# Kernel tuning notes

Measured on AMD Instinct MI355X. Metric: run time of the kernel, lower is better.

The kernel has to match this reference:

```python
import jax, jax.numpy as jnp
import numpy as np

B, S, D, H = 2, 2048, 1024, 16
HD = D // H  # head_dim = 64


def setup_inputs() -> dict:
    key = jax.random.key(0)
    ks = jax.random.split(key, 9)
    s = 1.0 / np.sqrt(D)
    return {
        "x": jax.random.normal(ks[0], (B, S, D), dtype=jnp.float32),
        "Wq": jax.random.uniform(ks[1], (D, D), jnp.float32, -s, s),
        "bq": jnp.zeros((D,), jnp.float32),
        "Wk": jax.random.uniform(ks[2], (D, D), jnp.float32, -s, s),
        "bk": jnp.zeros((D,), jnp.float32),
        "Wv": jax.random.uniform(ks[3], (D, D), jnp.float32, -s, s),
        "bv": jnp.zeros((D,), jnp.float32),
        "Wo": jax.random.uniform(ks[4], (D, D), jnp.float32, -s, s),
        "bo": jnp.zeros((D,), jnp.float32),
    }


def reference(x, Wq, bq, Wk, bk, Wv, bv, Wo, bo):
    # x: [B,S,D] -> Q/K/V: [B,H,S,HD]
    def heads(t):
        return t.reshape(B, S, H, HD).transpose(0, 2, 1, 3)

    Q = heads(x @ Wq + bq)
    K = heads(x @ Wk + bk)
    V = heads(x @ Wv + bv)
    scale = jnp.sqrt(jnp.asarray(HD, dtype=x.dtype))
    energy = jnp.einsum("bhqd,bhkd->bhqk", Q, K) / scale  # [B,H,S,S]
    attn = jax.nn.softmax(energy, axis=-1)
    # dropout is identity in eval mode
    o = jnp.einsum("bhqk,bhkd->bhqd", attn, V)  # [B,H,S,HD]
    o = o.transpose(0, 2, 1, 3).reshape(B, S, D)
    return o @ Wo + bo
```

## Files before the change

kernel.cpp:

```cpp
#include <hip/hip_runtime.h>
#include <hip/hip_bf16.h>

#define B_  2
#define S_  2048
#define D_  1024
#define H_  16
#define HD_ 64

typedef __attribute__((ext_vector_type(8))) short bf16x8;
typedef __attribute__((ext_vector_type(4))) float f32x4;

typedef __attribute__((address_space(1))) const short gbl_short;
typedef __attribute__((address_space(3))) short lds_short;

__device__ __forceinline__ short f2bf(float f) {
  union { float f; unsigned u; } v; v.f = f;
  unsigned r = (v.u + 0x7FFFu + ((v.u >> 16) & 1u)) >> 16;
  return (short)r;
}

__device__ __forceinline__ short bf16s(float f) {
  __hip_bfloat16 h = __float2bfloat16(f);
  return *reinterpret_cast<short*>(&h);
}

__global__ __launch_bounds__(256) void cast_x_kernel(const float* __restrict__ x,
                                                     short* __restrict__ xb) {
  int i = blockIdx.x * 256 + threadIdx.x;
  float4 v = ((const float4*)x)[i];
  short4 o;
  o.x = f2bf(v.x); o.y = f2bf(v.y); o.z = f2bf(v.z); o.w = f2bf(v.w);
  ((short4*)xb)[i] = o;
}

__global__ __launch_bounds__(256) void transpose_cast_w(
    const float* __restrict__ w0, const float* __restrict__ w1,
    const float* __restrict__ w2, const float* __restrict__ w3,
    short* __restrict__ t0, short* __restrict__ t1,
    short* __restrict__ t2, short* __restrict__ t3) {
  const float* W = blockIdx.z == 0 ? w0 : blockIdx.z == 1 ? w1 : blockIdx.z == 2 ? w2 : w3;
  short* T       = blockIdx.z == 0 ? t0 : blockIdx.z == 1 ? t1 : blockIdx.z == 2 ? t2 : t3;
  __shared__ float tile[32][33];
  int tx = threadIdx.x, ty = threadIdx.y;
  int x0 = blockIdx.x * 32, y0 = blockIdx.y * 32;
#pragma unroll
  for (int i = 0; i < 4; ++i)
    tile[ty + i * 8][tx] = W[(y0 + ty + i * 8) * D_ + x0 + tx];
  __syncthreads();
#pragma unroll
  for (int i = 0; i < 4; ++i)
    T[(x0 + ty + i * 8) * D_ + y0 + tx] = f2bf(tile[tx][ty + i * 8]);
}

__device__ __forceinline__ void gemm_mainloop64(
    const short* __restrict__ A, const short* __restrict__ Bt, int K,
    int m0, int n0, short* lA, short* lB, short* lA2, short* lB2,
    f32x4 acc[4][4], int lane, int wave) {
  const int l15 = lane & 15, quad = lane >> 4;
  const int wm = wave & 1, wn = wave >> 1;
  const int srow = lane >> 2;
  const int skp  = (lane & 3) * 8;

  for (int kk = 0; kk < K; kk += 64) {
#pragma unroll
    for (int j = 0; j < 2; ++j) {
      int c = wave * 2 + j;
      int row = c * 16 + srow;
      __builtin_amdgcn_global_load_lds(
          (gbl_short*)(A + (m0 + row) * K + kk + skp),
          (lds_short*)(lA + c * 512 + lane * 8), 16, 0, 0);
      __builtin_amdgcn_global_load_lds(
          (gbl_short*)(Bt + (n0 + row) * K + kk + skp),
          (lds_short*)(lB + c * 512 + lane * 8), 16, 0, 0);
      __builtin_amdgcn_global_load_lds(
          (gbl_short*)(A + (m0 + row) * K + kk + 32 + skp),
          (lds_short*)(lA2 + c * 512 + lane * 8), 16, 0, 0);
      __builtin_amdgcn_global_load_lds(
          (gbl_short*)(Bt + (n0 + row) * K + kk + 32 + skp),
          (lds_short*)(lB2 + c * 512 + lane * 8), 16, 0, 0);
    }
    __syncthreads();

    bf16x8 af[4], bf[4], af2[4], bf2[4];
#pragma unroll
    for (int i = 0; i < 4; ++i) {
      af[i]  = *(const bf16x8*)(lA  + (wm * 64 + i * 16 + l15) * 32 + quad * 8);
      bf[i]  = *(const bf16x8*)(lB  + (wn * 64 + i * 16 + l15) * 32 + quad * 8);
      af2[i] = *(const bf16x8*)(lA2 + (wm * 64 + i * 16 + l15) * 32 + quad * 8);
      bf2[i] = *(const bf16x8*)(lB2 + (wn * 64 + i * 16 + l15) * 32 + quad * 8);
    }
#pragma unroll
    for (int mi = 0; mi < 4; ++mi)
#pragma unroll
      for (int ni = 0; ni < 4; ++ni) {
        acc[mi][ni] = __builtin_amdgcn_mfma_f32_16x16x32_bf16(af[mi],  bf[ni],  acc[mi][ni], 0, 0, 0);
        acc[mi][ni] = __builtin_amdgcn_mfma_f32_16x16x32_bf16(af2[mi], bf2[ni], acc[mi][ni], 0, 0, 0);
      }
    __syncthreads();
  }
}

__global__ __launch_bounds__(256) void qkv_gemm(
    const short* __restrict__ xb,
    const short* __restrict__ Wqt, const short* __restrict__ Wkt, const short* __restrict__ Wvt,
    const float* __restrict__ bq, const float* __restrict__ bk, const float* __restrict__ bv,
    short* __restrict__ Qb, short* __restrict__ Kb, short* __restrict__ Vtb) {
  const int which = blockIdx.z;
  const short* Bt   = which == 0 ? Wqt : which == 1 ? Wkt : Wvt;
  const float* bias = which == 0 ? bq  : which == 1 ? bk  : bv;
  const float scl   = which == 0 ? 0.125f * 1.44269504089f : 1.0f;
  const int lane = threadIdx.x & 63, wave = threadIdx.x >> 6;
  const int l15 = lane & 15, quad = lane >> 4;
  const int wm = wave & 1, wn = wave >> 1;
  const int m0 = blockIdx.x * 128, n0 = blockIdx.y * 128;

  __shared__ short lA[128 * 32];
  __shared__ short lB[128 * 32];
  __shared__ short lA2[128 * 32];
  __shared__ short lB2[128 * 32];

  f32x4 acc[4][4];
#pragma unroll
  for (int mi = 0; mi < 4; ++mi)
#pragma unroll
    for (int ni = 0; ni < 4; ++ni) { f32x4 z = {0.f, 0.f, 0.f, 0.f}; acc[mi][ni] = z; }

  gemm_mainloop64(xb, Bt, D_, m0, n0, lA, lB, lA2, lB2, acc, lane, wave);

#pragma unroll
  for (int mi = 0; mi < 4; ++mi) {
    int m = m0 + wm * 64 + mi * 16 + quad * 4;
    int bb = m >> 11;
    int s0 = m & (S_ - 1);
#pragma unroll
    for (int ni = 0; ni < 4; ++ni) {
      int n = n0 + wn * 64 + ni * 16 + l15;
      int h = n >> 6, hd = n & 63;
      float bsv = bias[n];
      if (which < 2) {
        short* dst = which == 0 ? Qb : Kb;
#pragma unroll
        for (int r = 0; r < 4; ++r)
          dst[((bb * H_ + h) * S_ + (s0 + r)) * HD_ + hd] = f2bf((acc[mi][ni][r] + bsv) * scl);
      } else {
        short4 pk;
        pk.x = f2bf(acc[mi][ni][0] + bsv);
        pk.y = f2bf(acc[mi][ni][1] + bsv);
        pk.z = f2bf(acc[mi][ni][2] + bsv);
        pk.w = f2bf(acc[mi][ni][3] + bsv);
        *(short4*)(Vtb + ((bb * H_ + h) * HD_ + hd) * S_ + s0) = pk;
      }
    }
  }
}

__global__ __launch_bounds__(256) void out_gemm(
    const short* __restrict__ Ob, const short* __restrict__ Wot,
    const float* __restrict__ bo, float* __restrict__ out) {
  const int lane = threadIdx.x & 63, wave = threadIdx.x >> 6;
  const int l15 = lane & 15, quad = lane >> 4;
  const int m0 = blockIdx.x * 128, n0 = blockIdx.y * 64;
  const int srow = lane >> 2;
  const int skp  = (lane & 3) * 8;

  __shared__ short lA[128 * 32];
  __shared__ short lA2[128 * 32];
  __shared__ short lB[64 * 32];
  __shared__ short lB2[64 * 32];

  f32x4 acc[2][4];
#pragma unroll
  for (int mi = 0; mi < 2; ++mi)
#pragma unroll
    for (int ni = 0; ni < 4; ++ni) { f32x4 z = {0.f, 0.f, 0.f, 0.f}; acc[mi][ni] = z; }

  for (int kk = 0; kk < D_; kk += 64) {
#pragma unroll
    for (int j = 0; j < 2; ++j) {
      int c = wave * 2 + j;
      __builtin_amdgcn_global_load_lds(
          (gbl_short*)(Ob + (m0 + c * 16 + srow) * D_ + kk + skp),
          (lds_short*)(lA + c * 512 + lane * 8), 16, 0, 0);
      __builtin_amdgcn_global_load_lds(
          (gbl_short*)(Ob + (m0 + c * 16 + srow) * D_ + kk + 32 + skp),
          (lds_short*)(lA2 + c * 512 + lane * 8), 16, 0, 0);
    }
    __builtin_amdgcn_global_load_lds(
        (gbl_short*)(Wot + (n0 + wave * 16 + srow) * D_ + kk + skp),
        (lds_short*)(lB + wave * 512 + lane * 8), 16, 0, 0);
    __builtin_amdgcn_global_load_lds(
        (gbl_short*)(Wot + (n0 + wave * 16 + srow) * D_ + kk + 32 + skp),
        (lds_short*)(lB2 + wave * 512 + lane * 8), 16, 0, 0);
    __syncthreads();

    bf16x8 af[2], bf[4], af2[2], bf2[4];
#pragma unroll
    for (int i = 0; i < 2; ++i) {
      af[i]  = *(const bf16x8*)(lA  + (wave * 32 + i * 16 + l15) * 32 + quad * 8);
      af2[i] = *(const bf16x8*)(lA2 + (wave * 32 + i * 16 + l15) * 32 + quad * 8);
    }
#pragma unroll
    for (int i = 0; i < 4; ++i) {
      bf[i]  = *(const bf16x8*)(lB  + (i * 16 + l15) * 32 + quad * 8);
      bf2[i] = *(const bf16x8*)(lB2 + (i * 16 + l15) * 32 + quad * 8);
    }
#pragma unroll
    for (int mi = 0; mi < 2; ++mi)
#pragma unroll
      for (int ni = 0; ni < 4; ++ni) {
        acc[mi][ni] = __builtin_amdgcn_mfma_f32_16x16x32_bf16(af[mi],  bf[ni],  acc[mi][ni], 0, 0, 0);
        acc[mi][ni] = __builtin_amdgcn_mfma_f32_16x16x32_bf16(af2[mi], bf2[ni], acc[mi][ni], 0, 0, 0);
      }
    __syncthreads();
  }

#pragma unroll
  for (int mi = 0; mi < 2; ++mi) {
    int m = m0 + wave * 32 + mi * 16 + quad * 4;
#pragma unroll
    for (int ni = 0; ni < 4; ++ni) {
      int n = n0 + ni * 16 + l15;
      float bsv = bo[n];
#pragma unroll
      for (int r = 0; r < 4; ++r)
        out[(m + r) * D_ + n] = acc[mi][ni][r] + bsv;
    }
  }
}

__global__ __launch_bounds__(512, 4) void attn_kernel(
    const short* __restrict__ Qb, const short* __restrict__ Kb,
    const short* __restrict__ Vtb, short* __restrict__ Ob) {
  const int qt = blockIdx.x, h = blockIdx.y, b = blockIdx.z;
  const int base = (b * H_ + h) * S_ * HD_;
  const int tid = threadIdx.x;
  const int lane = tid & 63, wave = tid >> 6;
  const int grp = wave >> 2;
  const int wq  = wave & 3;
  const int l15 = lane & 15, quad = lane >> 4;

  __shared__ __align__(16) short lK[2][64 * 64];
  __shared__ __align__(16) short lV[2][64 * 64];
  __shared__ __align__(16) short lP[8][32 * 88];

  const int q0 = qt * 128 + wq * 32;

  bf16x8 qf[2][2];
#pragma unroll
  for (int mi = 0; mi < 2; ++mi)
#pragma unroll
    for (int ks = 0; ks < 2; ++ks)
      qf[mi][ks] = *(const bf16x8*)(Qb + base + (q0 + mi * 16 + l15) * HD_ + ks * 32 + quad * 8);

  f32x4 oacc[2][4];
  f32x4 lacc[2];
#pragma unroll
  for (int mi = 0; mi < 2; ++mi) {
    f32x4 z = {0.f, 0.f, 0.f, 0.f};
    lacc[mi] = z;
#pragma unroll
    for (int nb = 0; nb < 4; ++nb) oacc[mi][nb] = z;
  }

  bf16x8 onesf;
#pragma unroll
  for (int i = 0; i < 8; ++i) onesf[i] = (short)0x3F80;

  const int tig  = tid & 255;
  const int slot = tig & 7;
  const int rbase = tig >> 3;
  const int sgrp = ((slot ^ (rbase & 7))) * 8;
  const short* kp = Kb + base + (grp * 1024 + rbase) * HD_ + sgrp;
  const short* vp = Vtb + base + rbase * S_ + grp * 1024 + sgrp;
  lds_short* ldk0 = (lds_short*)(&lK[grp][0] + tig * 8);
  lds_short* ldv0 = (lds_short*)(&lV[grp][0] + tig * 8);

  short* pw = &lP[wave][0];
  const int swz = l15 & 7;

  for (int kt = 0; kt < 16; ++kt) {
#pragma unroll
    for (int j = 0; j < 2; ++j) {
      __builtin_amdgcn_global_load_lds((gbl_short*)(kp + j * 32 * HD_), ldk0 + j * 2048, 16, 0, 0);
      __builtin_amdgcn_global_load_lds((gbl_short*)(vp + j * 32 * S_),  ldv0 + j * 2048, 16, 0, 0);
    }
    kp += 64 * HD_;
    vp += 64;
    __syncthreads();

    f32x4 sacc[2][4];
#pragma unroll
    for (int mi = 0; mi < 2; ++mi)
#pragma unroll
      for (int nb = 0; nb < 4; ++nb) { f32x4 z = {0.f, 0.f, 0.f, 0.f}; sacc[mi][nb] = z; }
#pragma unroll
    for (int nb = 0; nb < 4; ++nb)
#pragma unroll
      for (int ks = 0; ks < 2; ++ks) {
        bf16x8 kf = *(const bf16x8*)(&lK[grp][0] + (nb * 16 + l15) * 64 + (((ks * 4 + quad) ^ swz) * 8));
        sacc[0][nb] = __builtin_amdgcn_mfma_f32_16x16x32_bf16(qf[0][ks], kf, sacc[0][nb], 0, 0, 0);
        sacc[1][nb] = __builtin_amdgcn_mfma_f32_16x16x32_bf16(qf[1][ks], kf, sacc[1][nb], 0, 0, 0);
      }

#pragma unroll
    for (int mi = 0; mi < 2; ++mi)
#pragma unroll
      for (int nb = 0; nb < 4; ++nb)
#pragma unroll
        for (int r = 0; r < 4; ++r)
          pw[(mi * 16 + quad * 4 + r) * 88 + nb * 16 + l15] =
              bf16s(__builtin_amdgcn_exp2f(sacc[mi][nb][r]));

    bf16x8 af[2][2];
#pragma unroll
    for (int mi = 0; mi < 2; ++mi)
#pragma unroll
      for (int ks = 0; ks < 2; ++ks)
        af[mi][ks] = *(const bf16x8*)(pw + (mi * 16 + l15) * 88 + ks * 32 + quad * 8);
#pragma unroll
    for (int nbh = 0; nbh < 4; ++nbh)
#pragma unroll
      for (int ks = 0; ks < 2; ++ks) {
        bf16x8 vf = *(const bf16x8*)(&lV[grp][0] + (nbh * 16 + l15) * 64 + (((ks * 4 + quad) ^ swz) * 8));
        oacc[0][nbh] = __builtin_amdgcn_mfma_f32_16x16x32_bf16(af[0][ks], vf, oacc[0][nbh], 0, 0, 0);
        oacc[1][nbh] = __builtin_amdgcn_mfma_f32_16x16x32_bf16(af[1][ks], vf, oacc[1][nbh], 0, 0, 0);
      }
#pragma unroll
    for (int mi = 0; mi < 2; ++mi) {
      lacc[mi] = __builtin_amdgcn_mfma_f32_16x16x32_bf16(af[mi][0], onesf, lacc[mi], 0, 0, 0);
      lacc[mi] = __builtin_amdgcn_mfma_f32_16x16x32_bf16(af[mi][1], onesf, lacc[mi], 0, 0, 0);
    }
    __syncthreads();
  }

  float* exch = (float*)(&lP[0][0]);
  float* lex  = exch + 4 * 2048;
  if (grp == 1) {
#pragma unroll
    for (int mi = 0; mi < 2; ++mi)
#pragma unroll
      for (int nbh = 0; nbh < 4; ++nbh)
#pragma unroll
        for (int r = 0; r < 4; ++r)
          exch[wq * 2048 + (mi * 16 + quad * 4 + r) * 64 + nbh * 16 + l15] = oacc[mi][nbh][r];
    if (l15 == 0) {
#pragma unroll
      for (int mi = 0; mi < 2; ++mi)
#pragma unroll
        for (int r = 0; r < 4; ++r)
          lex[wq * 32 + mi * 16 + quad * 4 + r] = lacc[mi][r];
    }
  }
  __syncthreads();
  if (grp == 0) {
#pragma unroll
    for (int mi = 0; mi < 2; ++mi)
#pragma unroll
      for (int r = 0; r < 4; ++r) {
        int row = mi * 16 + quad * 4 + r;
        float l2 = lex[wq * 32 + row];
        float inv = 1.0f / (lacc[mi][r] + l2);
        int sg = q0 + row;
#pragma unroll
        for (int nbh = 0; nbh < 4; ++nbh) {
          float o2 = exch[wq * 2048 + row * 64 + nbh * 16 + l15];
          Ob[(b * S_ + sg) * D_ + h * HD_ + nbh * 16 + l15] =
              bf16s((oacc[mi][nbh][r] + o2) * inv);
        }
      }
  }
}

extern "C" void kernel_launch(void* const* d_in, const int* in_sizes, int n_in,
                              void* d_out, int out_size, void* d_ws, size_t ws_size,
                              hipStream_t stream) {
  (void)in_sizes; (void)n_in; (void)out_size; (void)ws_size;
  const float* x  = (const float*)d_in[0];
  const float* Wq = (const float*)d_in[1];
  const float* bq = (const float*)d_in[2];
  const float* Wk = (const float*)d_in[3];
  const float* bk = (const float*)d_in[4];
  const float* Wv = (const float*)d_in[5];
  const float* bv = (const float*)d_in[6];
  const float* Wo = (const float*)d_in[7];
  const float* bo = (const float*)d_in[8];
  float* out = (float*)d_out;

  char* ws = (char*)d_ws;
  short* xb  = (short*)(ws);
  short* Wqt = (short*)(ws + 8388608);
  short* Wkt = Wqt + 1048576;
  short* Wvt = Wkt + 1048576;
  short* Wot = Wvt + 1048576;
  short* Qb  = Wot + 1048576;
  short* Kb  = Qb + 4194304;
  short* Vtb = Kb + 4194304;
  short* Ob  = Vtb + 4194304;

  cast_x_kernel<<<4096, 256, 0, stream>>>(x, xb);
  transpose_cast_w<<<dim3(32, 32, 4), dim3(32, 8), 0, stream>>>(
      Wq, Wk, Wv, Wo, Wqt, Wkt, Wvt, Wot);
  qkv_gemm<<<dim3(32, 8, 3), 256, 0, stream>>>(
      xb, Wqt, Wkt, Wvt, bq, bk, bv, Qb, Kb, Vtb);
  attn_kernel<<<dim3(16, 16, 2), 512, 0, stream>>>(Qb, Kb, Vtb, Ob);
  out_gemm<<<dim3(32, 16), 256, 0, stream>>>(Ob, Wot, bo, out);
}
```

Measured before the change: 203.8 us.

## Double-buffer GEMM K-loops and shrink attention P scratch for higher occupancy

The QKV and output GEMMs move from a single-buffered 64-wide K step to a double-buffered 32-wide K step, so the global-to-LDS copy of the next tile overlaps the MFMAs on the current one. In the attention kernel the per-wave P scratch shrinks from 32x88 to 16x72 with an XOR swizzle and is reused per mi. The LDS arrays are merged into one 50 KB buffer and the launch bound is raised from 4 to 6 blocks per CU. This aims to hide load latency and fit more attention waves per CU. The risks are more barriers per K step in the GEMMs and register pressure from the tighter occupancy target.

```diff
diff --git a/kernel.cpp b/kernel.cpp
--- a/kernel.cpp
+++ b/kernel.cpp
@@ -50,54 +50,6 @@
 #pragma unroll
   for (int i = 0; i < 4; ++i)
     T[(x0 + ty + i * 8) * D_ + y0 + tx] = f2bf(tile[tx][ty + i * 8]);
-}
-
-__device__ __forceinline__ void gemm_mainloop64(
-    const short* __restrict__ A, const short* __restrict__ Bt, int K,
-    int m0, int n0, short* lA, short* lB, short* lA2, short* lB2,
-    f32x4 acc[4][4], int lane, int wave) {
-  const int l15 = lane & 15, quad = lane >> 4;
-  const int wm = wave & 1, wn = wave >> 1;
-  const int srow = lane >> 2;
-  const int skp  = (lane & 3) * 8;
-
-  for (int kk = 0; kk < K; kk += 64) {
-#pragma unroll
-    for (int j = 0; j < 2; ++j) {
-      int c = wave * 2 + j;
-      int row = c * 16 + srow;
-      __builtin_amdgcn_global_load_lds(
-          (gbl_short*)(A + (m0 + row) * K + kk + skp),
-          (lds_short*)(lA + c * 512 + lane * 8), 16, 0, 0);
-      __builtin_amdgcn_global_load_lds(
-          (gbl_short*)(Bt + (n0 + row) * K + kk + skp),
-          (lds_short*)(lB + c * 512 + lane * 8), 16, 0, 0);
-      __builtin_amdgcn_global_load_lds(
-          (gbl_short*)(A + (m0 + row) * K + kk + 32 + skp),
-          (lds_short*)(lA2 + c * 512 + lane * 8), 16, 0, 0);
-      __builtin_amdgcn_global_load_lds(
-          (gbl_short*)(Bt + (n0 + row) * K + kk + 32 + skp),
-          (lds_short*)(lB2 + c * 512 + lane * 8), 16, 0, 0);
-    }
-    __syncthreads();
-
-    bf16x8 af[4], bf[4], af2[4], bf2[4];
-#pragma unroll
-    for (int i = 0; i < 4; ++i) {
-      af[i]  = *(const bf16x8*)(lA  + (wm * 64 + i * 16 + l15) * 32 + quad * 8);
-      bf[i]  = *(const bf16x8*)(lB  + (wn * 64 + i * 16 + l15) * 32 + quad * 8);
-      af2[i] = *(const bf16x8*)(lA2 + (wm * 64 + i * 16 + l15) * 32 + quad * 8);
-      bf2[i] = *(const bf16x8*)(lB2 + (wn * 64 + i * 16 + l15) * 32 + quad * 8);
-    }
-#pragma unroll
-    for (int mi = 0; mi < 4; ++mi)
-#pragma unroll
-      for (int ni = 0; ni < 4; ++ni) {
-        acc[mi][ni] = __builtin_amdgcn_mfma_f32_16x16x32_bf16(af[mi],  bf[ni],  acc[mi][ni], 0, 0, 0);
-        acc[mi][ni] = __builtin_amdgcn_mfma_f32_16x16x32_bf16(af2[mi], bf2[ni], acc[mi][ni], 0, 0, 0);
-      }
-    __syncthreads();
-  }
 }
 
 __global__ __launch_bounds__(256) void qkv_gemm(
@@ -113,11 +65,11 @@
   const int l15 = lane & 15, quad = lane >> 4;
   const int wm = wave & 1, wn = wave >> 1;
   const int m0 = blockIdx.x * 128, n0 = blockIdx.y * 128;
-
-  __shared__ short lA[128 * 32];
-  __shared__ short lB[128 * 32];
-  __shared__ short lA2[128 * 32];
-  __shared__ short lB2[128 * 32];
+  const int srow = lane >> 2;
+  const int skp  = (lane & 3) * 8;
+
+  __shared__ short lA[2][128 * 32];
+  __shared__ short lB[2][128 * 32];
 
   f32x4 acc[4][4];
 #pragma unroll
@@ -125,7 +77,39 @@
 #pragma unroll
     for (int ni = 0; ni < 4; ++ni) { f32x4 z = {0.f, 0.f, 0.f, 0.f}; acc[mi][ni] = z; }
 
-  gemm_mainloop64(xb, Bt, D_, m0, n0, lA, lB, lA2, lB2, acc, lane, wave);
+  auto stage = [&](int it, int buf) {
+    int kk = it * 32;
+#pragma unroll
+    for (int j = 0; j < 2; ++j) {
+      int c = wave * 2 + j;
+      int row = c * 16 + srow;
+      __builtin_amdgcn_global_load_lds(
+          (gbl_short*)(xb + (m0 + row) * D_ + kk + skp),
+          (lds_short*)(&lA[buf][0] + c * 512 + lane * 8), 16, 0, 0);
+      __builtin_amdgcn_global_load_lds(
+          (gbl_short*)(Bt + (n0 + row) * D_ + kk + skp),
+          (lds_short*)(&lB[buf][0] + c * 512 + lane * 8), 16, 0, 0);
+    }
+  };
+
+  stage(0, 0);
+  __syncthreads();
+  for (int it = 0; it < 32; ++it) {
+    int cur = it & 1;
+    if (it < 31) stage(it + 1, cur ^ 1);
+    bf16x8 af[4], bf[4];
+#pragma unroll
+    for (int i = 0; i < 4; ++i) {
+      af[i] = *(const bf16x8*)(&lA[cur][0] + (wm * 64 + i * 16 + l15) * 32 + quad * 8);
+      bf[i] = *(const bf16x8*)(&lB[cur][0] + (wn * 64 + i * 16 + l15) * 32 + quad * 8);
+    }
+#pragma unroll
+    for (int mi = 0; mi < 4; ++mi)
+#pragma unroll
+      for (int ni = 0; ni < 4; ++ni)
+        acc[mi][ni] = __builtin_amdgcn_mfma_f32_16x16x32_bf16(af[mi], bf[ni], acc[mi][ni], 0, 0, 0);
+    if (it < 31) __syncthreads();
+  }
 
 #pragma unroll
   for (int mi = 0; mi < 4; ++mi) {
@@ -163,10 +147,8 @@
   const int srow = lane >> 2;
   const int skp  = (lane & 3) * 8;
 
-  __shared__ short lA[128 * 32];
-  __shared__ short lA2[128 * 32];
-  __shared__ short lB[64 * 32];
-  __shared__ short lB2[64 * 32];
+  __shared__ short lA[2][128 * 32];
+  __shared__ short lB[2][64 * 32];
 
   f32x4 acc[2][4];
 #pragma unroll
@@ -174,44 +156,38 @@
 #pragma unroll
     for (int ni = 0; ni < 4; ++ni) { f32x4 z = {0.f, 0.f, 0.f, 0.f}; acc[mi][ni] = z; }
 
-  for (int kk = 0; kk < D_; kk += 64) {
+  auto stage = [&](int it, int buf) {
+    int kk = it * 32;
 #pragma unroll
     for (int j = 0; j < 2; ++j) {
       int c = wave * 2 + j;
       __builtin_amdgcn_global_load_lds(
           (gbl_short*)(Ob + (m0 + c * 16 + srow) * D_ + kk + skp),
-          (lds_short*)(lA + c * 512 + lane * 8), 16, 0, 0);
-      __builtin_amdgcn_global_load_lds(
-          (gbl_short*)(Ob + (m0 + c * 16 + srow) * D_ + kk + 32 + skp),
-          (lds_short*)(lA2 + c * 512 + lane * 8), 16, 0, 0);
+          (lds_short*)(&lA[buf][0] + c * 512 + lane * 8), 16, 0, 0);
     }
     __builtin_amdgcn_global_load_lds(
         (gbl_short*)(Wot + (n0 + wave * 16 + srow) * D_ + kk + skp),
-        (lds_short*)(lB + wave * 512 + lane * 8), 16, 0, 0);
-    __builtin_amdgcn_global_load_lds(
-        (gbl_short*)(Wot + (n0 + wave * 16 + srow) * D_ + kk + 32 + skp),
-        (lds_short*)(lB2 + wave * 512 + lane * 8), 16, 0, 0);
-    __syncthreads();
-
-    bf16x8 af[2], bf[4], af2[2], bf2[4];
-#pragma unroll
-    for (int i = 0; i < 2; ++i) {
-      af[i]  = *(const bf16x8*)(lA  + (wave * 32 + i * 16 + l15) * 32 + quad * 8);
-      af2[i] = *(const bf16x8*)(lA2 + (wave * 32 + i * 16 + l15) * 32 + quad * 8);
-    }
-#pragma unroll
-    for (int i = 0; i < 4; ++i) {
-      bf[i]  = *(const bf16x8*)(lB  + (i * 16 + l15) * 32 + quad * 8);
-      bf2[i] = *(const bf16x8*)(lB2 + (i * 16 + l15) * 32 + quad * 8);
-    }
+        (lds_short*)(&lB[buf][0] + wave * 512 + lane * 8), 16, 0, 0);
+  };
+
+  stage(0, 0);
+  __syncthreads();
+  for (int it = 0; it < 32; ++it) {
+    int cur = it & 1;
+    if (it < 31) stage(it + 1, cur ^ 1);
+    bf16x8 af[2], bf[4];
+#pragma unroll
+    for (int i = 0; i < 2; ++i)
+      af[i] = *(const bf16x8*)(&lA[cur][0] + (wave * 32 + i * 16 + l15) * 32 + quad * 8);
+#pragma unroll
+    for (int i = 0; i < 4; ++i)
+      bf[i] = *(const bf16x8*)(&lB[cur][0] + (i * 16 + l15) * 32 + quad * 8);
 #pragma unroll
     for (int mi = 0; mi < 2; ++mi)
 #pragma unroll
-      for (int ni = 0; ni < 4; ++ni) {
-        acc[mi][ni] = __builtin_amdgcn_mfma_f32_16x16x32_bf16(af[mi],  bf[ni],  acc[mi][ni], 0, 0, 0);
-        acc[mi][ni] = __builtin_amdgcn_mfma_f32_16x16x32_bf16(af2[mi], bf2[ni], acc[mi][ni], 0, 0, 0);
-      }
-    __syncthreads();
+      for (int ni = 0; ni < 4; ++ni)
+        acc[mi][ni] = __builtin_amdgcn_mfma_f32_16x16x32_bf16(af[mi], bf[ni], acc[mi][ni], 0, 0, 0);
+    if (it < 31) __syncthreads();
   }
 
 #pragma unroll
@@ -228,7 +204,7 @@
   }
 }
 
-__global__ __launch_bounds__(512, 4) void attn_kernel(
+__global__ __launch_bounds__(512, 6) void attn_kernel(
     const short* __restrict__ Qb, const short* __restrict__ Kb,
     const short* __restrict__ Vtb, short* __restrict__ Ob) {
   const int qt = blockIdx.x, h = blockIdx.y, b = blockIdx.z;
@@ -239,9 +215,10 @@
   const int wq  = wave & 3;
   const int l15 = lane & 15, quad = lane >> 4;
 
-  __shared__ __align__(16) short lK[2][64 * 64];
-  __shared__ __align__(16) short lV[2][64 * 64];
-  __shared__ __align__(16) short lP[8][32 * 88];
+  __shared__ __align__(16) char smem[51200];
+  short* lK  = (short*)smem;
+  short* lV  = (short*)(smem + 16384);
+  short* lPw = (short*)(smem + 32768);
 
   const int q0 = qt * 128 + wq * 32;
 
@@ -272,10 +249,11 @@
   const int sgrp = ((slot ^ (rbase & 7))) * 8;
   const short* kp = Kb + base + (grp * 1024 + rbase) * HD_ + sgrp;
   const short* vp = Vtb + base + rbase * S_ + grp * 1024 + sgrp;
-  lds_short* ldk0 = (lds_short*)(&lK[grp][0] + tig * 8);
-  lds_short* ldv0 = (lds_short*)(&lV[grp][0] + tig * 8);
-
-  short* pw = &lP[wave][0];
+  lds_short* ldk0 = (lds_short*)(lK + grp * 4096 + tig * 8);
+  lds_short* ldv0 = (lds_short*)(lV + grp * 4096 + tig * 8);
+
+  short* pw = lPw + wave * 1152;
+  short* pbase = pw + quad * 4 * 72;
   const int swz = l15 & 7;
 
   for (int kt = 0; kt < 16; ++kt) {
@@ -297,31 +275,32 @@
     for (int nb = 0; nb < 4; ++nb)
 #pragma unroll
       for (int ks = 0; ks < 2; ++ks) {
-        bf16x8 kf = *(const bf16x8*)(&lK[grp][0] + (nb * 16 + l15) * 64 + (((ks * 4 + quad) ^ swz) * 8));
+        bf16x8 kf = *(const bf16x8*)(lK + grp * 4096 + (nb * 16 + l15) * 64 + (((ks * 4 + quad) ^ swz) * 8));
         sacc[0][nb] = __builtin_amdgcn_mfma_f32_16x16x32_bf16(qf[0][ks], kf, sacc[0][nb], 0, 0, 0);
         sacc[1][nb] = __builtin_amdgcn_mfma_f32_16x16x32_bf16(qf[1][ks], kf, sacc[1][nb], 0, 0, 0);
       }
 
-#pragma unroll
-    for (int mi = 0; mi < 2; ++mi)
-#pragma unroll
-      for (int nb = 0; nb < 4; ++nb)
+    bf16x8 af[2][2];
+#pragma unroll
+    for (int mi = 0; mi < 2; ++mi) {
+#pragma unroll
+      for (int nb = 0; nb < 4; ++nb) {
+        int cofs = ((nb ^ quad) * 16) + l15;
 #pragma unroll
         for (int r = 0; r < 4; ++r)
-          pw[(mi * 16 + quad * 4 + r) * 88 + nb * 16 + l15] =
-              bf16s(__builtin_amdgcn_exp2f(sacc[mi][nb][r]));
-
-    bf16x8 af[2][2];
-#pragma unroll
-    for (int mi = 0; mi < 2; ++mi)
+          pbase[r * 72 + cofs] = bf16s(__builtin_amdgcn_exp2f(sacc[mi][nb][r]));
+      }
 #pragma unroll
       for (int ks = 0; ks < 2; ++ks)
-        af[mi][ks] = *(const bf16x8*)(pw + (mi * 16 + l15) * 88 + ks * 32 + quad * 8);
+        af[mi][ks] = *(const bf16x8*)(pw + l15 * 72 +
+            (((ks * 2 + (quad >> 1)) ^ (l15 >> 2)) * 16) + (quad & 1) * 8);
+    }
+
 #pragma unroll
     for (int nbh = 0; nbh < 4; ++nbh)
 #pragma unroll
       for (int ks = 0; ks < 2; ++ks) {
-        bf16x8 vf = *(const bf16x8*)(&lV[grp][0] + (nbh * 16 + l15) * 64 + (((ks * 4 + quad) ^ swz) * 8));
+        bf16x8 vf = *(const bf16x8*)(lV + grp * 4096 + (nbh * 16 + l15) * 64 + (((ks * 4 + quad) ^ swz) * 8));
         oacc[0][nbh] = __builtin_amdgcn_mfma_f32_16x16x32_bf16(af[0][ks], vf, oacc[0][nbh], 0, 0, 0);
         oacc[1][nbh] = __builtin_amdgcn_mfma_f32_16x16x32_bf16(af[1][ks], vf, oacc[1][nbh], 0, 0, 0);
       }
@@ -333,8 +312,8 @@
     __syncthreads();
   }
 
-  float* exch = (float*)(&lP[0][0]);
-  float* lex  = exch + 4 * 2048;
+  float* exch = (float*)smem;
+  float* lex  = (float*)(smem + 32768);
   if (grp == 1) {
 #pragma unroll
     for (int mi = 0; mi < 2; ++mi)
```

After: 320.8 us. 1.57x slower.
